# Kernel tuning notes

Hardware: AMD Instinct MI355X
Metric: run time of the kernel (lower is better)

The kernel has to match this reference:

```python
import jax, jax.numpy as jnp
import numpy as np

TEMP = 0.5
EPS = 1e-12  # torch F.normalize eps


def setup_inputs() -> dict:
    key = jax.random.key(0)
    k1, k2, k3 = jax.random.split(key, 3)
    B, D = 2048, 128
    z = jax.random.normal(k1, (B, D), dtype=jnp.float32)
    z_aug = jax.random.normal(k2, (B, D), dtype=jnp.float32)
    labels = jax.random.randint(k3, (B,), 0, 2, dtype=jnp.int64)
    return {"z": z, "z_aug": z_aug, "labels": labels}


def _l2_normalize(x):
    n = jnp.linalg.norm(x, axis=1, keepdims=True)
    return x / jnp.maximum(n, EPS)


def _pucon_loss(z, z_aug, labels):
    B = z.shape[0]
    z = _l2_normalize(z)
    z_aug = _l2_normalize(z_aug)

    s00 = (z @ z.T) / TEMP          # [B, B]
    s01 = (z @ z_aug.T) / TEMP
    s10 = (z_aug @ z.T) / TEMP
    s11 = (z_aug @ z_aug.T) / TEMP

    eye = jnp.eye(B, dtype=bool)

    # ---- SelfSupConLoss (reduction='none'): CE over rows with own-diagonal
    # removed from the 00/11 blocks; removal == masking with -inf for CE.
    neg_inf = jnp.array(-jnp.inf, dtype=s00.dtype)
    logits = jnp.concatenate([
        jnp.concatenate([s01, jnp.where(eye, neg_inf, s00)], axis=1),
        jnp.concatenate([s10, jnp.where(eye, neg_inf, s11)], axis=1),
    ], axis=0)                       # [2B, 2B]
    pos = jnp.concatenate([jnp.diagonal(s01), jnp.diagonal(s10)])  # [2B]
    lse = jax.scipy.special.logsumexp(logits, axis=1)
    unsup = lse - pos                # [2B] per-sample NT-Xent loss

    # ---- SupConLoss (reduction='none')
    M = jnp.concatenate([
        jnp.concatenate([s00, s01], axis=1),
        jnp.concatenate([s10, s11], axis=1),
    ], axis=0)                       # [2B, 2B]
    mx = jax.lax.stop_gradient(jnp.max(M, axis=1, keepdims=True))
    Ms = M - mx
    mask = ~jnp.eye(2 * B, dtype=bool)
    e = jnp.where(mask, jnp.exp(Ms), 0.0)
    denom = jnp.sum(e, axis=1, keepdims=True)
    # -log(exp(Ms)/denom) on off-diagonal entries, 0 on diagonal
    nll = jnp.where(mask, jnp.log(denom) - Ms, 0.0)
    eq = labels[:, None] == labels[None, :]
    eq2 = jnp.tile(eq, (2, 2))       # [2B, 2B] bool
    sup = jnp.sum(nll * eq2, axis=1) / (jnp.sum(eq2, axis=1) - 1)  # [2B]

    # ---- PU combination: positives use sup loss, unlabeled use unsup loss
    lab2 = jnp.tile(labels, 2)       # [2B]
    pos_m = (lab2 == 1)
    neg_m = (lab2 == 0)
    n_p = jnp.sum(pos_m)
    n_u = jnp.sum(neg_m)
    total = jnp.maximum(n_p + n_u, 1)
    loss = (jnp.sum(jnp.where(pos_m, sup, 0.0)) +
            jnp.sum(jnp.where(neg_m, unsup, 0.0))) / total
    return jnp.where(n_p == 0, jnp.mean(unsup), loss)


def reference(z, z_aug, labels):
    return _pucon_loss(z, z_aug, labels)
```

## Files before the change

### kernel.cpp

```cpp
#include <hip/hip_runtime.h>
#include <hip/hip_bf16.h>

#define Bsz 2048
#define Dim 128
#define Nrows 4096

typedef float f32x4 __attribute__((ext_vector_type(4)));
typedef __bf16 bf16x8 __attribute__((ext_vector_type(8)));

#define GLD_LDS16(gp, lp)                                                        \
    __builtin_amdgcn_global_load_lds(                                            \
        (const __attribute__((address_space(1))) void*)(gp),                     \
        (__attribute__((address_space(3))) void*)(lp), 16, 0, 0)


__global__ __launch_bounds__(256) void k_norm(const float* __restrict__ z,
                                              const float* __restrict__ za,
                                              const long long* __restrict__ labels,
                                              __bf16* __restrict__ U,
                                              int* __restrict__ c1out) {
    const int wid = threadIdx.x >> 6, lane = threadIdx.x & 63;
    #pragma unroll
    for (int pass = 0; pass < 4; pass++) {
        const int r = blockIdx.x * 16 + pass * 4 + wid;
        const float* src = (r < Bsz) ? (z + (size_t)r * Dim) : (za + (size_t)(r - Bsz) * Dim);
        float2 x = reinterpret_cast<const float2*>(src)[lane];
        float ss = x.x * x.x + x.y * x.y;
        #pragma unroll
        for (int m = 1; m < 64; m <<= 1) ss += __shfl_xor(ss, m);
        const float sc = 1.0f / fmaxf(sqrtf(ss), 1e-12f);
        __bf16* dst = U + (size_t)r * Dim + 2 * lane;
        dst[0] = (__bf16)(x.x * sc);
        dst[1] = (__bf16)(x.y * sc);
    }
    if (blockIdx.x == 0) {
        __shared__ int ci[256];
        const int t = threadIdx.x;
        int c = 0;
        #pragma unroll
        for (int k = 0; k < 8; k++) c += (int)labels[t * 8 + k];
        ci[t] = c;
        __syncthreads();
        for (int s = 128; s > 0; s >>= 1) {
            if (t < s) ci[t] += ci[t + s];
            __syncthreads();
        }
        if (t == 0) c1out[0] = ci[0];
    }
}

__global__ __launch_bounds__(256, 4) void k_gram(const __bf16* __restrict__ U,
                                                 const long long* __restrict__ labels,
                                                 float* __restrict__ part,
                                                 float* __restrict__ rs1p,
                                                 float* __restrict__ rsap,
                                                 float* __restrict__ dpv) {
    __shared__ __bf16 Aj[128 * 128];

    const int iblk = blockIdx.x >> 5, jblk = blockIdx.x & 31;
    const int ibase = iblk * 128, jbase = jblk * 128;
    const int w = threadIdx.x >> 6, lane = threadIdx.x & 63;
    const int wi = w & 1, wj = w >> 1;
    const int l15 = lane & 15, l4 = lane >> 4;

    bf16x8 b[4][4];
    #pragma unroll
    for (int bt = 0; bt < 4; bt++)
        #pragma unroll
        for (int ks = 0; ks < 4; ks++)
            b[bt][ks] = *reinterpret_cast<const bf16x8*>(
                U + (size_t)(ibase + wi * 64 + bt * 16 + l15) * Dim + (ks * 4 + l4) * 8);

    {
        const int c = lane & 15, rsub = lane >> 4;
        #pragma unroll
        for (int it = 0; it < 8; it++) {
            const int rl = w * 32 + it * 4 + rsub;
            const __bf16* src = U + (size_t)(jbase + rl) * Dim + ((c ^ (rl & 7)) * 8);
            GLD_LDS16(src, Aj + (size_t)(w * 32 + it * 4) * 128);
        }
    }

    const unsigned long long lmask =
        __ballot(labels[(jbase + wj * 64 + lane) & (Bsz - 1)] == 1);

    __syncthreads();

    float dsum[4] = {0.f, 0.f, 0.f, 0.f};
    float r1s[4]  = {0.f, 0.f, 0.f, 0.f};
    float ras[4]  = {0.f, 0.f, 0.f, 0.f};
    const float KE1 = 2.8853900817779268f;
    const float KE0 = -2.8853900817779268f;

    #pragma unroll
    for (int at = 0; at < 4; at++) {
        const int rlb = wj * 64 + at * 16 + l15;
        bf16x8 a[4];
        #pragma unroll
        for (int ks = 0; ks < 4; ks++)
            a[ks] = *reinterpret_cast<const bf16x8*>(
                Aj + (size_t)rlb * 128 + (((ks * 4 + l4) ^ (rlb & 7)) * 8));
        float labq[4];
        #pragma unroll
        for (int q = 0; q < 4; q++)
            labq[q] = (float)((lmask >> (at * 16 + l4 * 4 + q)) & 1ull);
        const int jt = jbase + wj * 64 + at * 16;

        #pragma unroll
        for (int bt = 0; bt < 4; bt++) {
            f32x4 acc = {0.f, 0.f, 0.f, 0.f};
            #pragma unroll
            for (int ks = 0; ks < 4; ks++)
                acc = __builtin_amdgcn_mfma_f32_16x16x32_bf16(a[ks], b[bt][ks], acc, 0, 0, 0);
            const int itl = ibase + wi * 64 + bt * 16;
            const bool dg = (jt == itl);
            const bool pg = (jt == (itl ^ 2048));
            #pragma unroll
            for (int q = 0; q < 4; q++) {
                float av = acc[q];
                const bool sel = (l15 == l4 * 4 + q);
                if (pg && sel) dpv[itl + l15] = av;
                float e = exp2f(fmaf(av, KE1, KE0));
                if (dg && sel) { e = 0.f; av = 0.f; }
                dsum[bt] += e;
                ras[bt] += av;
                r1s[bt] = fmaf(labq[q], av, r1s[bt]);
            }
        }
    }

    const int strip = jblk * 2 + wj;
    #pragma unroll
    for (int bt = 0; bt < 4; bt++) {
        float v0 = dsum[bt], v1 = r1s[bt], v2 = ras[bt];
        v0 += __shfl_xor(v0, 16); v0 += __shfl_xor(v0, 32);
        v1 += __shfl_xor(v1, 16); v1 += __shfl_xor(v1, 32);
        v2 += __shfl_xor(v2, 16); v2 += __shfl_xor(v2, 32);
        if (l4 == 0) {
            const int row = ibase + wi * 64 + bt * 16 + l15;
            part[row * 64 + strip] = v0;
            rs1p[row * 64 + strip] = v1;
            rsap[row * 64 + strip] = v2;
        }
    }
}

__global__ __launch_bounds__(256) void k_row(const long long* __restrict__ labels,
                                             const int* __restrict__ c1p,
                                             const float* __restrict__ part,
                                             const float* __restrict__ rs1p,
                                             const float* __restrict__ rsap,
                                             const float* __restrict__ dpv,
                                             float* __restrict__ rowC,
                                             float* __restrict__ rowU) {
    const int wid = threadIdx.x >> 6, lane = threadIdx.x & 63;
    const int c1 = *c1p;
    float cs = 0.f, us = 0.f;
    #pragma unroll
    for (int rr = 0; rr < 4; rr++) {
        const int i = blockIdx.x * 16 + wid * 4 + rr;
        float dn = part[i * 64 + lane];
        float v1 = rs1p[i * 64 + lane];
        float va = rsap[i * 64 + lane];
        #pragma unroll
        for (int m = 1; m < 64; m <<= 1) {
            dn += __shfl_xor(dn, m);
            v1 += __shfl_xor(v1, m);
            va += __shfl_xor(va, m);
        }
        if (lane == 0) {
            const long long lb = labels[i & (Bsz - 1)];
            const float lnD = logf(dn) + 2.0f;
            const float uns = lnD - 2.0f * dpv[i];
            const float cnt = 2.f * (float)((lb == 1) ? c1 : (Bsz - c1));
            const float sumeq = 2.f * ((lb == 1) ? v1 : (va - v1));
            const float sup = lnD - sumeq / (cnt - 1.f);
            cs += (lb == 1) ? sup : uns;
            us += uns;
        }
    }
    __shared__ float wcs[4], wus[4];
    if (lane == 0) { wcs[wid] = cs; wus[wid] = us; }
    __syncthreads();
    if (threadIdx.x == 0) {
        rowC[blockIdx.x] = wcs[0] + wcs[1] + wcs[2] + wcs[3];
        rowU[blockIdx.x] = wus[0] + wus[1] + wus[2] + wus[3];
    }
}

__global__ __launch_bounds__(256) void k_comb(const float* __restrict__ rowC,
                                              const float* __restrict__ rowU,
                                              const int* __restrict__ c1p,
                                              float* __restrict__ out) {
    __shared__ float sc[256], su[256];
    const int t = threadIdx.x;
    sc[t] = rowC[t];
    su[t] = rowU[t];
    __syncthreads();
    for (int s = 128; s > 0; s >>= 1) {
        if (t < s) { sc[t] += sc[t + s]; su[t] += su[t + s]; }
        __syncthreads();
    }
    if (t == 0) out[0] = ((*c1p > 0) ? sc[0] : su[0]) / (float)Nrows;
}

extern "C" void kernel_launch(void* const* d_in, const int* in_sizes, int n_in,
                              void* d_out, int out_size, void* d_ws, size_t ws_size,
                              hipStream_t stream) {
    const float* z  = (const float*)d_in[0];
    const float* za = (const float*)d_in[1];
    const long long* labels = (const long long*)d_in[2];

    char* ws = (char*)d_ws;
    __bf16* U    = (__bf16*)(ws);
    float*  part = (float*)(ws + (1u << 20));
    float*  rs1p = (float*)(ws + (2u << 20));
    float*  rsap = (float*)(ws + (3u << 20));
    float*  dpv  = (float*)(ws + (4u << 20));
    float*  rowC = (float*)(ws + (4u << 20) + (16u << 10));
    float*  rowU = (float*)(ws + (4u << 20) + (17u << 10));
    int*    c1   = (int*)  (ws + (4u << 20) + (18u << 10));
    float*  out  = (float*)d_out;

    hipLaunchKernelGGL(k_norm, dim3(256),  dim3(256), 0, stream, z, za, labels, U, c1);
    hipLaunchKernelGGL(k_gram, dim3(1024), dim3(256), 0, stream, U, labels, part, rs1p, rsap, dpv);
    hipLaunchKernelGGL(k_row,  dim3(256),  dim3(256), 0, stream, labels, c1, part, rs1p, rsap, dpv, rowC, rowU);
    hipLaunchKernelGGL(k_comb, dim3(1),    dim3(256), 0, stream, rowC, rowU, c1, out);
}
```

Measured before the change: 36.99 us.

## Replace label-weighted gram row sums with dot products against class-sum vectors

Row sums of similarities restricted to same-label columns are rewritten by linearity: each row dots with a per-class sum of normalized vectors, which the norm kernel builds as per-block partials and an extra block of the gram kernel reduces. The gram epilogue now keeps only the exp-sum accumulator, dropping the two extra accumulators, two partial writes and the positive-pair diagonal store, and it stages the i-tile in LDS alongside the j-tile. The positive-pair and self terms are recomputed in the row kernel from the bf16 vectors. The cost is twice the shared memory per block, occupancy hint lowered to 2, and slight numeric differences from subtracting the self term.

```diff
diff --git a/kernel.cpp b/kernel.cpp
--- a/kernel.cpp
+++ b/kernel.cpp
@@ -18,8 +18,13 @@
                                               const float* __restrict__ za,
                                               const long long* __restrict__ labels,
                                               __bf16* __restrict__ U,
+                                              float* __restrict__ w1p,
+                                              float* __restrict__ wallp,
                                               int* __restrict__ c1out) {
     const int wid = threadIdx.x >> 6, lane = threadIdx.x & 63;
+    __shared__ float s1[4][128];
+    __shared__ float s0[4][128];
+    float a1x = 0.f, a1y = 0.f, a0x = 0.f, a0y = 0.f;
     #pragma unroll
     for (int pass = 0; pass < 4; pass++) {
         const int r = blockIdx.x * 16 + pass * 4 + wid;
@@ -29,13 +34,24 @@
         #pragma unroll
         for (int m = 1; m < 64; m <<= 1) ss += __shfl_xor(ss, m);
         const float sc = 1.0f / fmaxf(sqrtf(ss), 1e-12f);
+        const float u0 = x.x * sc, u1 = x.y * sc;
         __bf16* dst = U + (size_t)r * Dim + 2 * lane;
-        dst[0] = (__bf16)(x.x * sc);
-        dst[1] = (__bf16)(x.y * sc);
+        dst[0] = (__bf16)u0;
+        dst[1] = (__bf16)u1;
+        const float lf = (labels[r & (Bsz - 1)] == 1) ? 1.f : 0.f;
+        a0x += u0; a0y += u1;
+        a1x = fmaf(lf, u0, a1x); a1y = fmaf(lf, u1, a1y);
+    }
+    s1[wid][2 * lane] = a1x; s1[wid][2 * lane + 1] = a1y;
+    s0[wid][2 * lane] = a0x; s0[wid][2 * lane + 1] = a0y;
+    __syncthreads();
+    const int t = threadIdx.x;
+    if (t < 128) {
+        w1p[blockIdx.x * 128 + t]   = s1[0][t] + s1[1][t] + s1[2][t] + s1[3][t];
+        wallp[blockIdx.x * 128 + t] = s0[0][t] + s0[1][t] + s0[2][t] + s0[3][t];
     }
     if (blockIdx.x == 0) {
         __shared__ int ci[256];
-        const int t = threadIdx.x;
         int c = 0;
         #pragma unroll
         for (int k = 0; k < 8; k++) c += (int)labels[t * 8 + k];
@@ -49,12 +65,24 @@
     }
 }
 
-__global__ __launch_bounds__(256, 4) void k_gram(const __bf16* __restrict__ U,
-                                                 const long long* __restrict__ labels,
+__global__ __launch_bounds__(256, 2) void k_gram(const __bf16* __restrict__ U,
+                                                 const float* __restrict__ w1p,
+                                                 const float* __restrict__ wallp,
                                                  float* __restrict__ part,
-                                                 float* __restrict__ rs1p,
-                                                 float* __restrict__ rsap,
-                                                 float* __restrict__ dpv) {
+                                                 float* __restrict__ w1,
+                                                 float* __restrict__ wall) {
+    if (blockIdx.x == 1024) {
+        const int t = threadIdx.x;
+        const int d = t & 127;
+        const float* src = (t < 128) ? w1p : wallp;
+        float acc = 0.f;
+        #pragma unroll 8
+        for (int k = 0; k < 256; k++) acc += src[k * 128 + d];
+        if (t < 128) w1[d] = acc; else wall[d] = acc;
+        return;
+    }
+
+    __shared__ __bf16 Ai[128 * 128];
     __shared__ __bf16 Aj[128 * 128];
 
     const int iblk = blockIdx.x >> 5, jblk = blockIdx.x & 31;
@@ -63,47 +91,37 @@
     const int wi = w & 1, wj = w >> 1;
     const int l15 = lane & 15, l4 = lane >> 4;
 
+    {
+        const int c = lane & 15, rsub = lane >> 4;
+        #pragma unroll
+        for (int it = 0; it < 8; it++) {
+            const int rl = w * 32 + it * 4 + rsub;
+            const int soff = (c ^ (rl & 7)) * 8;
+            GLD_LDS16(U + (size_t)(ibase + rl) * Dim + soff, Ai + (size_t)(w * 32 + it * 4) * 128);
+            GLD_LDS16(U + (size_t)(jbase + rl) * Dim + soff, Aj + (size_t)(w * 32 + it * 4) * 128);
+        }
+    }
+    __syncthreads();
+
     bf16x8 b[4][4];
     #pragma unroll
     for (int bt = 0; bt < 4; bt++)
         #pragma unroll
         for (int ks = 0; ks < 4; ks++)
             b[bt][ks] = *reinterpret_cast<const bf16x8*>(
-                U + (size_t)(ibase + wi * 64 + bt * 16 + l15) * Dim + (ks * 4 + l4) * 8);
-
-    {
-        const int c = lane & 15, rsub = lane >> 4;
-        #pragma unroll
-        for (int it = 0; it < 8; it++) {
-            const int rl = w * 32 + it * 4 + rsub;
-            const __bf16* src = U + (size_t)(jbase + rl) * Dim + ((c ^ (rl & 7)) * 8);
-            GLD_LDS16(src, Aj + (size_t)(w * 32 + it * 4) * 128);
-        }
-    }
-
-    const unsigned long long lmask =
-        __ballot(labels[(jbase + wj * 64 + lane) & (Bsz - 1)] == 1);
-
-    __syncthreads();
+                Ai + ((wi * 64 + bt * 16 + l15) * 16 + ((ks * 4 + l4) ^ (l15 & 7))) * 8);
 
     float dsum[4] = {0.f, 0.f, 0.f, 0.f};
-    float r1s[4]  = {0.f, 0.f, 0.f, 0.f};
-    float ras[4]  = {0.f, 0.f, 0.f, 0.f};
     const float KE1 = 2.8853900817779268f;
     const float KE0 = -2.8853900817779268f;
 
     #pragma unroll
     for (int at = 0; at < 4; at++) {
-        const int rlb = wj * 64 + at * 16 + l15;
         bf16x8 a[4];
         #pragma unroll
         for (int ks = 0; ks < 4; ks++)
             a[ks] = *reinterpret_cast<const bf16x8*>(
-                Aj + (size_t)rlb * 128 + (((ks * 4 + l4) ^ (rlb & 7)) * 8));
-        float labq[4];
-        #pragma unroll
-        for (int q = 0; q < 4; q++)
-            labq[q] = (float)((lmask >> (at * 16 + l4 * 4 + q)) & 1ull);
+                Aj + ((wj * 64 + at * 16 + l15) * 16 + ((ks * 4 + l4) ^ (l15 & 7))) * 8);
         const int jt = jbase + wj * 64 + at * 16;
 
         #pragma unroll
@@ -112,19 +130,12 @@
             #pragma unroll
             for (int ks = 0; ks < 4; ks++)
                 acc = __builtin_amdgcn_mfma_f32_16x16x32_bf16(a[ks], b[bt][ks], acc, 0, 0, 0);
-            const int itl = ibase + wi * 64 + bt * 16;
-            const bool dg = (jt == itl);
-            const bool pg = (jt == (itl ^ 2048));
+            const bool dg = (jt == ibase + wi * 64 + bt * 16);
             #pragma unroll
             for (int q = 0; q < 4; q++) {
-                float av = acc[q];
-                const bool sel = (l15 == l4 * 4 + q);
-                if (pg && sel) dpv[itl + l15] = av;
-                float e = exp2f(fmaf(av, KE1, KE0));
-                if (dg && sel) { e = 0.f; av = 0.f; }
+                float e = exp2f(fmaf(acc[q], KE1, KE0));
+                if (dg && (l15 == l4 * 4 + q)) e = 0.f;
                 dsum[bt] += e;
-                ras[bt] += av;
-                r1s[bt] = fmaf(labq[q], av, r1s[bt]);
             }
         }
     }
@@ -132,48 +143,55 @@
     const int strip = jblk * 2 + wj;
     #pragma unroll
     for (int bt = 0; bt < 4; bt++) {
-        float v0 = dsum[bt], v1 = r1s[bt], v2 = ras[bt];
-        v0 += __shfl_xor(v0, 16); v0 += __shfl_xor(v0, 32);
-        v1 += __shfl_xor(v1, 16); v1 += __shfl_xor(v1, 32);
-        v2 += __shfl_xor(v2, 16); v2 += __shfl_xor(v2, 32);
-        if (l4 == 0) {
-            const int row = ibase + wi * 64 + bt * 16 + l15;
-            part[row * 64 + strip] = v0;
-            rs1p[row * 64 + strip] = v1;
-            rsap[row * 64 + strip] = v2;
-        }
-    }
-}
-
-__global__ __launch_bounds__(256) void k_row(const long long* __restrict__ labels,
+        float v0 = dsum[bt];
+        v0 += __shfl_xor(v0, 16);
+        v0 += __shfl_xor(v0, 32);
+        if (l4 == 0)
+            part[(ibase + wi * 64 + bt * 16 + l15) * 64 + strip] = v0;
+    }
+}
+
+__global__ __launch_bounds__(256) void k_row(const __bf16* __restrict__ U,
+                                             const long long* __restrict__ labels,
                                              const int* __restrict__ c1p,
                                              const float* __restrict__ part,
-                                             const float* __restrict__ rs1p,
-                                             const float* __restrict__ rsap,
-                                             const float* __restrict__ dpv,
+                                             const float* __restrict__ w1,
+                                             const float* __restrict__ wall,
                                              float* __restrict__ rowC,
                                              float* __restrict__ rowU) {
     const int wid = threadIdx.x >> 6, lane = threadIdx.x & 63;
     const int c1 = *c1p;
+    const float w1a = w1[2 * lane], w1b = w1[2 * lane + 1];
+    const float wa  = wall[2 * lane], wb = wall[2 * lane + 1];
     float cs = 0.f, us = 0.f;
     #pragma unroll
     for (int rr = 0; rr < 4; rr++) {
         const int i = blockIdx.x * 16 + wid * 4 + rr;
+        const int partner = (i < Bsz) ? i + Bsz : i - Bsz;
         float dn = part[i * 64 + lane];
-        float v1 = rs1p[i * 64 + lane];
-        float va = rsap[i * 64 + lane];
+        const float u0 = (float)U[(size_t)i * Dim + 2 * lane];
+        const float u1 = (float)U[(size_t)i * Dim + 2 * lane + 1];
+        const float p0 = (float)U[(size_t)partner * Dim + 2 * lane];
+        const float p1 = (float)U[(size_t)partner * Dim + 2 * lane + 1];
+        float d1 = u0 * w1a + u1 * w1b;
+        float da = u0 * wa + u1 * wb;
+        float ds = u0 * u0 + u1 * u1;
+        float dp = u0 * p0 + u1 * p1;
         #pragma unroll
         for (int m = 1; m < 64; m <<= 1) {
             dn += __shfl_xor(dn, m);
-            v1 += __shfl_xor(v1, m);
-            va += __shfl_xor(va, m);
+            d1 += __shfl_xor(d1, m);
+            da += __shfl_xor(da, m);
+            ds += __shfl_xor(ds, m);
+            dp += __shfl_xor(dp, m);
         }
         if (lane == 0) {
             const long long lb = labels[i & (Bsz - 1)];
             const float lnD = logf(dn) + 2.0f;
-            const float uns = lnD - 2.0f * dpv[i];
+            const float uns = lnD - 2.0f * dp;
             const float cnt = 2.f * (float)((lb == 1) ? c1 : (Bsz - c1));
-            const float sumeq = 2.f * ((lb == 1) ? v1 : (va - v1));
+            const float sii = 2.f * ds;
+            const float sumeq = ((lb == 1) ? 2.f * d1 : 2.f * (da - d1)) - sii;
             const float sup = lnD - sumeq / (cnt - 1.f);
             cs += (lb == 1) ? sup : uns;
             us += uns;
@@ -212,18 +230,19 @@
     const long long* labels = (const long long*)d_in[2];
 
     char* ws = (char*)d_ws;
-    __bf16* U    = (__bf16*)(ws);
-    float*  part = (float*)(ws + (1u << 20));
-    float*  rs1p = (float*)(ws + (2u << 20));
-    float*  rsap = (float*)(ws + (3u << 20));
-    float*  dpv  = (float*)(ws + (4u << 20));
-    float*  rowC = (float*)(ws + (4u << 20) + (16u << 10));
-    float*  rowU = (float*)(ws + (4u << 20) + (17u << 10));
-    int*    c1   = (int*)  (ws + (4u << 20) + (18u << 10));
-    float*  out  = (float*)d_out;
-
-    hipLaunchKernelGGL(k_norm, dim3(256),  dim3(256), 0, stream, z, za, labels, U, c1);
-    hipLaunchKernelGGL(k_gram, dim3(1024), dim3(256), 0, stream, U, labels, part, rs1p, rsap, dpv);
-    hipLaunchKernelGGL(k_row,  dim3(256),  dim3(256), 0, stream, labels, c1, part, rs1p, rsap, dpv, rowC, rowU);
+    __bf16* U     = (__bf16*)(ws);
+    float*  part  = (float*)(ws + (1u << 20));
+    float*  w1p   = (float*)(ws + (2u << 20));
+    float*  wallp = (float*)(ws + (2u << 20) + (128u << 10));
+    float*  w1    = (float*)(ws + (2u << 20) + (256u << 10));
+    float*  wall  = (float*)(ws + (2u << 20) + (256u << 10) + 512);
+    int*    c1    = (int*)  (ws + (2u << 20) + (256u << 10) + 1024);
+    float*  rowC  = (float*)(ws + (2u << 20) + (257u << 10));
+    float*  rowU  = (float*)(ws + (2u << 20) + (258u << 10));
+    float*  out   = (float*)d_out;
+
+    hipLaunchKernelGGL(k_norm, dim3(256),  dim3(256), 0, stream, z, za, labels, U, w1p, wallp, c1);
+    hipLaunchKernelGGL(k_gram, dim3(1025), dim3(256), 0, stream, U, w1p, wallp, part, w1, wall);
+    hipLaunchKernelGGL(k_row,  dim3(256),  dim3(256), 0, stream, U, labels, c1, part, w1, wall, rowC, rowU);
     hipLaunchKernelGGL(k_comb, dim3(1),    dim3(256), 0, stream, rowC, rowU, c1, out);
 }
```

New measurement: 34.23 us. -7.5%, faster.
